# Optimization experiments

Measured on AMD Instinct MI355X. Metric: run time of the kernel, lower is better.

## Reference

```python
import jax, jax.numpy as jnp
import numpy as np

H = 5          # hidden size
D = 178        # input size


def setup_inputs() -> dict:
    key = jax.random.key(0)
    ks = jax.random.split(key, 8)
    B, T = 2048, 512
    s = 1.0 / np.sqrt(H)  # torch LSTM/Linear init scale
    x = jax.random.normal(ks[0], (B, T, D), dtype=jnp.float32)
    w_ih = jax.random.uniform(ks[1], (4 * H, D), jnp.float32, -s, s)
    w_hh = jax.random.uniform(ks[2], (4 * H, H), jnp.float32, -s, s)
    b_ih = jax.random.uniform(ks[3], (4 * H,), jnp.float32, -s, s)
    b_hh = jax.random.uniform(ks[4], (4 * H,), jnp.float32, -s, s)
    w_fc = jax.random.uniform(ks[5], (H, H), jnp.float32, -s, s)
    b_fc = jax.random.uniform(ks[6], (H,), jnp.float32, -s, s)
    return {"x": x, "w_ih": w_ih, "w_hh": w_hh, "b_ih": b_ih,
            "b_hh": b_hh, "w_fc": w_fc, "b_fc": b_fc}


def _lstm_last_h(x, w_ih, w_hh, b_ih, b_hh):
    # x: (B, T, D). PyTorch gate order: i, f, g, o along the 4H axis.
    B = x.shape[0]
    xg = jnp.einsum('btd,gd->tbg', x, w_ih) + b_ih  # (T, B, 4H) input-to-gate, precomputed
    h0 = jnp.zeros((B, H), x.dtype)
    c0 = jnp.zeros((B, H), x.dtype)

    def step(carry, gx):
        h, c = carry
        g = gx + h @ w_hh.T + b_hh            # (B, 4H)
        i, f, gg, o = jnp.split(g, 4, axis=-1)
        i = jax.nn.sigmoid(i)
        f = jax.nn.sigmoid(f)
        gg = jnp.tanh(gg)
        o = jax.nn.sigmoid(o)
        c = f * c + i * gg
        h = o * jnp.tanh(c)
        return (h, c), None

    (h, _c), _ = jax.lax.scan(step, (h0, c0), xg)
    return h  # (B, H) == output[:, -1]


def reference(x, w_ih, w_hh, b_ih, b_hh, w_fc, b_fc):
    h = _lstm_last_h(x, w_ih, w_hh, b_ih, b_hh)[:, None, :]  # (B, 1, H)
    return jax.nn.relu(h) @ w_fc.T + b_fc                    # (B, 1, H)
```

## Files before the change

### kernel.cpp

```cpp
#include <hip/hip_runtime.h>
#include <math.h>

#define B 2048
#define T 512
#define D 178
#define H 5
#define G 20

#define TILE 64
#define XS_STRIDE 180

__global__ __launch_bounds__(256) void proj_kernel(
    const float* __restrict__ x, const float* __restrict__ w_ih,
    const float* __restrict__ b_ih, const float* __restrict__ b_hh,
    float* __restrict__ xg)
{
    __shared__ __align__(16) float xs[TILE * XS_STRIDE];
    __shared__ __align__(16) float ws[G * XS_STRIDE];
    __shared__ float bs[G];

    const int tid = threadIdx.x;
    const int rt0 = blockIdx.x * TILE;
    const int t   = rt0 >> 11;
    const int b0  = rt0 & (B - 1);

    for (int idx = tid; idx < G * D; idx += 256) {
        int g = idx / D, d = idx - g * D;
        ws[g * XS_STRIDE + d] = w_ih[idx];
    }
    if (tid < G) bs[tid] = b_ih[tid] + b_hh[tid];

    {
        const int lane = tid & 63;
        const int q    = tid >> 6;
        const int row  = q * 16 + (lane >> 2);
        const int dg   = lane & 3;
        const float* xrow = x + ((size_t)(b0 + row) * T + t) * D;
        float* xsr = &xs[row * XS_STRIDE];
        #pragma unroll
        for (int i = 0; i < 23; ++i) {
            int d = dg * 2 + i * 8;
            if (d < D) {
                float2 v = *(const float2*)(xrow + d);
                xsr[d]     = v.x;
                xsr[d + 1] = v.y;
            }
        }
    }
    __syncthreads();

    const int j  = tid >> 2;
    const int gg = tid & 3;
    float acc[5];
    #pragma unroll
    for (int gi = 0; gi < 5; ++gi) acc[gi] = bs[gg * 5 + gi];

    const float* xr = &xs[j * XS_STRIDE];
    const float* wr = &ws[gg * 5 * XS_STRIDE];
    #pragma unroll 4
    for (int i = 0; i < 44; ++i) {
        float4 xv = *(const float4*)(xr + 4 * i);
        #pragma unroll
        for (int gi = 0; gi < 5; ++gi) {
            float4 wv = *(const float4*)(wr + gi * XS_STRIDE + 4 * i);
            acc[gi] += xv.x * wv.x + xv.y * wv.y + xv.z * wv.z + xv.w * wv.w;
        }
    }
    {
        float2 xv = *(const float2*)(xr + 176);
        #pragma unroll
        for (int gi = 0; gi < 5; ++gi) {
            float2 wv = *(const float2*)(wr + gi * XS_STRIDE + 176);
            acc[gi] += xv.x * wv.x + xv.y * wv.y;
        }
    }

    size_t base = (size_t)t * G * B + b0 + j;
    #pragma unroll
    for (int gi = 0; gi < 5; ++gi)
        xg[base + (size_t)(gg * 5 + gi) * B] = acc[gi];
}

__device__ __forceinline__ float frcp(float v) { return __builtin_amdgcn_rcpf(v); }
__device__ __forceinline__ float sigm(float v) { return frcp(1.f + __expf(-v)); }
__device__ __forceinline__ float tanh_fast(float v) {
    float e = __expf(-2.f * v);
    return (1.f - e) * frcp(1.f + e);
}

#define CH 8
#define GPB 12

__global__ __launch_bounds__(64) void scan_kernel(
    const float* __restrict__ xg, const float* __restrict__ w_hh,
    const float* __restrict__ w_fc, const float* __restrict__ b_fc,
    float* __restrict__ out)
{
    const int lane = threadIdx.x;
    int grp = lane / 5;
    int k   = lane - grp * 5;
    bool valid = (grp < GPB);
    if (!valid) { grp = 0; k = 0; }
    int b = blockIdx.x * GPB + grp;
    bool active = valid && (b < B);
    int bb = active ? b : 0;

    float whh[4][5];
    #pragma unroll
    for (int r = 0; r < 4; ++r)
        #pragma unroll
        for (int jj = 0; jj < 5; ++jj)
            whh[r][jj] = w_hh[(k + 5 * r) * H + jj];
    float wfc[5];
    #pragma unroll
    for (int jj = 0; jj < 5; ++jj) wfc[jj] = w_fc[k * H + jj];
    const float bfc = b_fc[k];

    float h[5] = {0.f, 0.f, 0.f, 0.f, 0.f};
    float c = 0.f;
    const int srcbase = grp * 5;

    const float* gbase = xg + (size_t)k * B + bb;

    float cur[CH][4], nxt[CH][4];
    #pragma unroll
    for (int s = 0; s < CH; ++s)
        #pragma unroll
        for (int r = 0; r < 4; ++r)
            cur[s][r] = gbase[(size_t)s * (G * B) + (size_t)r * (H * B)];

    for (int ch = 0; ch < T / CH; ++ch) {
        if (ch + 1 < T / CH) {
            const float* nb = gbase + (size_t)(ch + 1) * CH * (G * B);
            #pragma unroll
            for (int s = 0; s < CH; ++s)
                #pragma unroll
                for (int r = 0; r < 4; ++r)
                    nxt[s][r] = nb[(size_t)s * (G * B) + (size_t)r * (H * B)];
        }
        #pragma unroll
        for (int s = 0; s < CH; ++s) {
            float gi_ = cur[s][0], gf_ = cur[s][1], gg_ = cur[s][2], go_ = cur[s][3];
            #pragma unroll
            for (int jj = 0; jj < 5; ++jj) {
                gi_ += whh[0][jj] * h[jj];
                gf_ += whh[1][jj] * h[jj];
                gg_ += whh[2][jj] * h[jj];
                go_ += whh[3][jj] * h[jj];
            }
            float iv = sigm(gi_);
            float fv = sigm(gf_);
            float ov = sigm(go_);
            float gv = tanh_fast(gg_);
            c = fv * c + iv * gv;
            float hk = ov * tanh_fast(c);
            #pragma unroll
            for (int jj = 0; jj < 5; ++jj)
                h[jj] = __shfl(hk, srcbase + jj, 64);
        }
        #pragma unroll
        for (int s = 0; s < CH; ++s)
            #pragma unroll
            for (int r = 0; r < 4; ++r)
                cur[s][r] = nxt[s][r];
    }

    float o = bfc;
    #pragma unroll
    for (int jj = 0; jj < 5; ++jj)
        o += fmaxf(h[jj], 0.f) * wfc[jj];
    if (active) out[(size_t)b * H + k] = o;
}

extern "C" void kernel_launch(void* const* d_in, const int* in_sizes, int n_in,
                              void* d_out, int out_size, void* d_ws, size_t ws_size,
                              hipStream_t stream)
{
    const float* x    = (const float*)d_in[0];
    const float* w_ih = (const float*)d_in[1];
    const float* w_hh = (const float*)d_in[2];
    const float* b_ih = (const float*)d_in[3];
    const float* b_hh = (const float*)d_in[4];
    const float* w_fc = (const float*)d_in[5];
    const float* b_fc = (const float*)d_in[6];
    float* out = (float*)d_out;
    float* xg  = (float*)d_ws;

    proj_kernel<<<(B * T) / TILE, 256, 0, stream>>>(x, w_ih, b_ih, b_hh, xg);
    scan_kernel<<<(B + GPB - 1) / GPB, 64, 0, stream>>>(xg, w_hh, w_fc, b_fc, out);
}
```

Before: 1.176 ms.

## Read gate weights via wave-uniform scalar loads and reorder xg layout for coalesced scan reads

The projection kernel no longer stages w_ih in shared memory. Each wavefront now owns one gate group, which is made wave-uniform with readfirstlane, so weight reads can become scalar loads while each lane handles one row. The xg intermediate is relaid as (t, gate, b, k) so that the scan kernel's five lanes per batch read contiguous addresses. This removes LDS weight traffic and the weight-staging loop, and makes the scan loads more contiguous. In exchange, each lane now computes 5 outputs per row with 4 waves sharing the x tile, and the projection kernel's stores become strided by 5.

```diff
diff --git a/kernel.cpp b/kernel.cpp
--- a/kernel.cpp
+++ b/kernel.cpp
@@ -16,19 +16,11 @@
     float* __restrict__ xg)
 {
     __shared__ __align__(16) float xs[TILE * XS_STRIDE];
-    __shared__ __align__(16) float ws[G * XS_STRIDE];
-    __shared__ float bs[G];
 
     const int tid = threadIdx.x;
     const int rt0 = blockIdx.x * TILE;
     const int t   = rt0 >> 11;
     const int b0  = rt0 & (B - 1);
-
-    for (int idx = tid; idx < G * D; idx += 256) {
-        int g = idx / D, d = idx - g * D;
-        ws[g * XS_STRIDE + d] = w_ih[idx];
-    }
-    if (tid < G) bs[tid] = b_ih[tid] + b_hh[tid];
 
     {
         const int lane = tid & 63;
@@ -49,36 +41,37 @@
     }
     __syncthreads();
 
-    const int j  = tid >> 2;
-    const int gg = tid & 3;
+    const int lane = tid & 63;
+    const int r    = __builtin_amdgcn_readfirstlane(tid >> 6);
+    const float* wb = w_ih + (size_t)r * 5 * D;
+
     float acc[5];
     #pragma unroll
-    for (int gi = 0; gi < 5; ++gi) acc[gi] = bs[gg * 5 + gi];
+    for (int k = 0; k < 5; ++k)
+        acc[k] = b_ih[r * 5 + k] + b_hh[r * 5 + k];
 
-    const float* xr = &xs[j * XS_STRIDE];
-    const float* wr = &ws[gg * 5 * XS_STRIDE];
+    const float* xr = &xs[lane * XS_STRIDE];
     #pragma unroll 4
     for (int i = 0; i < 44; ++i) {
         float4 xv = *(const float4*)(xr + 4 * i);
         #pragma unroll
-        for (int gi = 0; gi < 5; ++gi) {
-            float4 wv = *(const float4*)(wr + gi * XS_STRIDE + 4 * i);
-            acc[gi] += xv.x * wv.x + xv.y * wv.y + xv.z * wv.z + xv.w * wv.w;
+        for (int k = 0; k < 5; ++k) {
+            const float* wp = wb + k * D + 4 * i;
+            acc[k] += xv.x * wp[0] + xv.y * wp[1] + xv.z * wp[2] + xv.w * wp[3];
         }
     }
     {
         float2 xv = *(const float2*)(xr + 176);
         #pragma unroll
-        for (int gi = 0; gi < 5; ++gi) {
-            float2 wv = *(const float2*)(wr + gi * XS_STRIDE + 176);
-            acc[gi] += xv.x * wv.x + xv.y * wv.y;
+        for (int k = 0; k < 5; ++k) {
+            const float* wp = wb + k * D + 176;
+            acc[k] += xv.x * wp[0] + xv.y * wp[1];
         }
     }
 
-    size_t base = (size_t)t * G * B + b0 + j;
+    float* o = xg + (((size_t)t * 4 + r) * B + (b0 + lane)) * 5;
     #pragma unroll
-    for (int gi = 0; gi < 5; ++gi)
-        xg[base + (size_t)(gg * 5 + gi) * B] = acc[gi];
+    for (int k = 0; k < 5; ++k) o[k] = acc[k];
 }
 
 __device__ __forceinline__ float frcp(float v) { return __builtin_amdgcn_rcpf(v); }
@@ -107,10 +100,10 @@
 
     float whh[4][5];
     #pragma unroll
-    for (int r = 0; r < 4; ++r)
+    for (int rr = 0; rr < 4; ++rr)
         #pragma unroll
         for (int jj = 0; jj < 5; ++jj)
-            whh[r][jj] = w_hh[(k + 5 * r) * H + jj];
+            whh[rr][jj] = w_hh[(k + 5 * rr) * H + jj];
     float wfc[5];
     #pragma unroll
     for (int jj = 0; jj < 5; ++jj) wfc[jj] = w_fc[k * H + jj];
@@ -120,23 +113,25 @@
     float c = 0.f;
     const int srcbase = grp * 5;
 
-    const float* gbase = xg + (size_t)k * B + bb;
+    const float* gb = xg + (size_t)bb * 5 + k;
+    const size_t TS = (size_t)4 * B * 5;
+    const size_t RS = (size_t)B * 5;
 
     float cur[CH][4], nxt[CH][4];
     #pragma unroll
     for (int s = 0; s < CH; ++s)
         #pragma unroll
-        for (int r = 0; r < 4; ++r)
-            cur[s][r] = gbase[(size_t)s * (G * B) + (size_t)r * (H * B)];
+        for (int rr = 0; rr < 4; ++rr)
+            cur[s][rr] = gb[(size_t)s * TS + (size_t)rr * RS];
 
     for (int ch = 0; ch < T / CH; ++ch) {
         if (ch + 1 < T / CH) {
-            const float* nb = gbase + (size_t)(ch + 1) * CH * (G * B);
+            const float* nb = gb + (size_t)(ch + 1) * CH * TS;
             #pragma unroll
             for (int s = 0; s < CH; ++s)
                 #pragma unroll
-                for (int r = 0; r < 4; ++r)
-                    nxt[s][r] = nb[(size_t)s * (G * B) + (size_t)r * (H * B)];
+                for (int rr = 0; rr < 4; ++rr)
+                    nxt[s][rr] = nb[(size_t)s * TS + (size_t)rr * RS];
         }
         #pragma unroll
         for (int s = 0; s < CH; ++s) {
@@ -161,8 +156,8 @@
         #pragma unroll
         for (int s = 0; s < CH; ++s)
             #pragma unroll
-            for (int r = 0; r < 4; ++r)
-                cur[s][r] = nxt[s][r];
+            for (int rr = 0; rr < 4; ++rr)
+                cur[s][rr] = nxt[s][rr];
     }
 
     float o = bfc;
```

Result: faster. 1.075 ms (-8.6%).
